# Kernel optimization log

Measured on AMD Instinct MI355X. Metric: run time of the kernel, lower is better.

Reference implementation:

```python
import jax, jax.numpy as jnp
import numpy as np

N = 100000   # nodes
E = 1600000  # edges (avg degree 16)
D = 128      # input_dim = hidden_dim = output_dim


def setup_inputs() -> dict:
    key = jax.random.key(0)
    ks = jax.random.split(key, 16)
    s = 0.02
    inp = {
        "node_emb": jax.random.normal(ks[0], (N, D), dtype=jnp.float32),
        "edge_index": jax.random.randint(ks[1], (2, E), 0, N, dtype=jnp.int64),
        # last-layer GCN branch (conv1 -> relu -> conv2); earlier layers are dead code in SSL.forward
        "gcn_w1": jax.random.normal(ks[2], (D, D), dtype=jnp.float32) * s,
        "gcn_b1": jnp.zeros((D,), dtype=jnp.float32),
        "gcn_w2": jax.random.normal(ks[3], (D, D), dtype=jnp.float32) * s,
        "gcn_b2": jnp.zeros((D,), dtype=jnp.float32),
        # last-layer GIN branch (GINConv eps=0, Mlp == single Linear)
        "gin_w1": jax.random.normal(ks[4], (D, D), dtype=jnp.float32) * s,
        "gin_b1": jnp.zeros((D,), dtype=jnp.float32),
        "gin_w2": jax.random.normal(ks[5], (D, D), dtype=jnp.float32) * s,
        "gin_b2": jnp.zeros((D,), dtype=jnp.float32),
        # fusion heads
        "lin_w": jax.random.normal(ks[6], (D, D), dtype=jnp.float32) * s,
        "lin_b": jnp.zeros((D,), dtype=jnp.float32),
        "fc_w": jax.random.normal(ks[7], (D, D), dtype=jnp.float32) * s,
        "fc_b": jnp.zeros((D,), dtype=jnp.float32),
    }
    return inp


def reference(node_emb, edge_index, gcn_w1, gcn_b1, gcn_w2, gcn_b2,
              gin_w1, gin_b1, gin_w2, gin_b2, lin_w, lin_b, fc_w, fc_b):
    n = node_emb.shape[0]
    src, dst = edge_index[0], edge_index[1]

    # symmetric GCN normalization with self-loops: deg counts incoming edges + 1
    deg = jax.ops.segment_sum(jnp.ones(src.shape[0], node_emb.dtype), dst, num_segments=n) + 1.0
    dinv = jax.lax.rsqrt(deg)                  # deg >= 1 always
    edge_norm = dinv[src] * dinv[dst]          # [E]
    self_norm = dinv * dinv                    # [N] self-loop coefficient

    def gcn_conv(x, W, b):
        y = x @ W                                                        # [N, D]
        agg = jax.ops.segment_sum(y[src] * edge_norm[:, None], dst, num_segments=n)
        return agg + self_norm[:, None] * y + b

    def gin_conv(x, W, b):
        # GINConv(train_eps=False): nn((1+0)*x + sum_{j in N(i)} x_j), nn = Linear
        agg = jax.ops.segment_sum(x[src], dst, num_segments=n)
        return (x + agg) @ W + b

    # GCN branch: conv1 -> relu -> (dropout=identity in eval) -> conv2
    h = jax.nn.relu(gcn_conv(node_emb, gcn_w1, gcn_b1))
    x_gcn = gcn_conv(h, gcn_w2, gcn_b2)

    # GIN branch: conv1 -> conv2
    g = gin_conv(node_emb, gin_w1, gin_b1)
    x_gin = gin_conv(g, gin_w2, gin_b2)

    # fusion heads
    x_gin = x_gin @ lin_w + lin_b
    x_gcn = x_gcn @ lin_w + lin_b
    return (x_gin + x_gcn) @ fc_w + fc_b
```

## Files before the change

### kernel.cpp

```cpp
#include <hip/hip_runtime.h>

#define D 128

using s8v = __attribute__((ext_vector_type(8))) short;
using f4v = __attribute__((ext_vector_type(4))) float;

__device__ __forceinline__ float bf2f(ushort u) {
  union { uint i; float f; } v; v.i = ((uint)u) << 16; return v.f;
}
__device__ __forceinline__ ushort f2bf(float f) {
  union { float f; uint i; } v; v.f = f;
  uint b = v.i;
  return (ushort)((b + 0x7fffu + ((b >> 16) & 1u)) >> 16);
}

__global__ void degpos_kernel(const int* __restrict__ dst, int* __restrict__ ideg,
                              int* __restrict__ pos, int E) {
  int i = blockIdx.x * blockDim.x + threadIdx.x;
  int stride = gridDim.x * blockDim.x;
  for (int e = i; e < E; e += stride)
    pos[e] = atomicAdd(&ideg[dst[e]], 1);
}

__global__ void scan1_kernel(const int* __restrict__ deg, int* __restrict__ incl,
                             int* __restrict__ bsum, int n) {
  __shared__ int tmp[256];
  int t = threadIdx.x;
  int i = blockIdx.x * 256 + t;
  int v = (i < n) ? deg[i] : 0;
  tmp[t] = v;
  __syncthreads();
#pragma unroll
  for (int off = 1; off < 256; off <<= 1) {
    int u = (t >= off) ? tmp[t - off] : 0;
    __syncthreads();
    tmp[t] += u;
    __syncthreads();
  }
  if (i < n) incl[i] = tmp[t];
  if (t == 255) bsum[blockIdx.x] = tmp[255];
}

__global__ void scan2_kernel(int* __restrict__ bsum, int nb) {
  __shared__ int tmp[256];
  __shared__ int carry_s;
  int t = threadIdx.x;
  if (t == 0) carry_s = 0;
  __syncthreads();
  for (int base = 0; base < nb; base += 256) {
    int v = (base + t < nb) ? bsum[base + t] : 0;
    tmp[t] = v;
    __syncthreads();
#pragma unroll
    for (int off = 1; off < 256; off <<= 1) {
      int u = (t >= off) ? tmp[t - off] : 0;
      __syncthreads();
      tmp[t] += u;
      __syncthreads();
    }
    int inc = tmp[t] + carry_s;
    if (base + t < nb) bsum[base + t] = inc;
    __syncthreads();
    if (t == 255) carry_s = inc;
    __syncthreads();
  }
}

__global__ void scan3_kernel(const int* __restrict__ deg, const int* __restrict__ incl,
                             const int* __restrict__ bsum, int* __restrict__ rowptr,
                             float* __restrict__ dinv, int n, int E) {
  int i = blockIdx.x * 256 + threadIdx.x;
  if (i < n) {
    int carry = (blockIdx.x > 0) ? bsum[blockIdx.x - 1] : 0;
    int d = deg[i];
    rowptr[i] = incl[i] - d + carry;
    dinv[i] = rsqrtf((float)d + 1.0f);
  }
  if (i == 0) rowptr[n] = E;
}

__global__ void scatter_kernel(const int* __restrict__ src, const int* __restrict__ dst,
                               const int* __restrict__ rowptr, const int* __restrict__ pos,
                               int* __restrict__ csrc, int E) {
  int i = blockIdx.x * blockDim.x + threadIdx.x;
  int stride = gridDim.x * blockDim.x;
  for (int e = i; e < E; e += stride)
    csrc[rowptr[dst[e]] + pos[e]] = src[e];
}

__global__ void xcvt_kernel(const float* __restrict__ x, ushort* __restrict__ xb, long total) {
  long i = ((long)blockIdx.x * blockDim.x + threadIdx.x) * 8;
  long stride = (long)gridDim.x * blockDim.x * 8;
  for (long t = i; t < total; t += stride) {
    float4 v0 = *(const float4*)(x + t);
    float4 v1 = *(const float4*)(x + t + 4);
    s8v u;
    u[0] = (short)f2bf(v0.x); u[1] = (short)f2bf(v0.y);
    u[2] = (short)f2bf(v0.z); u[3] = (short)f2bf(v0.w);
    u[4] = (short)f2bf(v1.x); u[5] = (short)f2bf(v1.y);
    u[6] = (short)f2bf(v1.z); u[7] = (short)f2bf(v1.w);
    *(s8v*)(xb + t) = u;
  }
}

__global__ void prep1_kernel(const float* __restrict__ gw1, const float* __restrict__ iw1,
                             ushort* __restrict__ Wt1g, ushort* __restrict__ Wt1i,
                             const float* __restrict__ lw, const float* __restrict__ fw,
                             float* __restrict__ LF) {
  int b = blockIdx.x;
  if (b < 128) {
    int t = b * 256 + threadIdx.x;
    int which = t >> 14, q = t & 16383;
    int k = q >> 7, c = q & 127;
    const float* w = which ? iw1 : gw1;
    ushort* o = which ? Wt1i : Wt1g;
    o[c * 128 + k] = f2bf(w[k * 128 + c]);
  } else {
    int t = (b - 128) * 256 + threadIdx.x;
    int r = t >> 7, c = t & 127;
    float s = 0.f;
#pragma unroll 8
    for (int k = 0; k < 128; ++k) s = fmaf(lw[r * 128 + k], fw[k * 128 + c], s);
    LF[r * 128 + c] = s;
  }
}

__global__ void prep2_kernel(const float* __restrict__ gw2, const float* __restrict__ iw2,
                             const float* __restrict__ LF,
                             ushort* __restrict__ Wt2g, ushort* __restrict__ Wt2i,
                             const float* __restrict__ gb2, const float* __restrict__ ib2,
                             const float* __restrict__ lb, const float* __restrict__ fw,
                             const float* __restrict__ fb, float* __restrict__ btot) {
  int b = blockIdx.x;
  if (b < 128) {
    int t = b * 256 + threadIdx.x;
    int which = t >> 14, q = t & 16383;
    int k = q >> 7, c = q & 127;
    const float* W = which ? iw2 : gw2;
    ushort* O = which ? Wt2i : Wt2g;
    float s = 0.f;
#pragma unroll 8
    for (int j = 0; j < 128; ++j) s = fmaf(W[k * 128 + j], LF[j * 128 + c], s);
    O[c * 128 + k] = f2bf(s);
  } else if (threadIdx.x < 128) {
    int c = threadIdx.x;
    float s = fb[c];
#pragma unroll 8
    for (int j = 0; j < 128; ++j) {
      s = fmaf(gb2[j] + ib2[j], LF[j * 128 + c], s);
      s = fmaf(2.f * lb[j], fw[j * 128 + c], s);
    }
    btot[c] = s;
  }
}

__global__ __launch_bounds__(256) void gatherA_kernel(
    const ushort* __restrict__ xb, const float* __restrict__ dinv,
    const int* __restrict__ rowptr, const int* __restrict__ csrc,
    ushort* __restrict__ ab, int n) {
  int nd = blockIdx.x * 4 + (threadIdx.x >> 6);
  if (nd >= n) return;
  int lane = threadIdx.x & 63;
  int half = lane >> 5;
  int hl = lane & 31;
  int beg = rowptr[nd], end = rowptr[nd + 1];
  float4 sg = make_float4(0.f, 0.f, 0.f, 0.f);
  float4 sc = make_float4(0.f, 0.f, 0.f, 0.f);
  int j = beg + half;
  for (; j + 6 < end; j += 8) {
    int s0 = csrc[j], s1 = csrc[j + 2], s2 = csrc[j + 4], s3 = csrc[j + 6];
    float w0 = dinv[s0], w1 = dinv[s1], w2 = dinv[s2], w3 = dinv[s3];
    ushort4 v0 = *(const ushort4*)(xb + (long)s0 * D + 4 * hl);
    ushort4 v1 = *(const ushort4*)(xb + (long)s1 * D + 4 * hl);
    ushort4 v2 = *(const ushort4*)(xb + (long)s2 * D + 4 * hl);
    ushort4 v3 = *(const ushort4*)(xb + (long)s3 * D + 4 * hl);
    float a0 = bf2f(v0.x), a1 = bf2f(v0.y), a2 = bf2f(v0.z), a3 = bf2f(v0.w);
    sg.x += a0; sg.y += a1; sg.z += a2; sg.w += a3;
    sc.x = fmaf(w0, a0, sc.x); sc.y = fmaf(w0, a1, sc.y);
    sc.z = fmaf(w0, a2, sc.z); sc.w = fmaf(w0, a3, sc.w);
    a0 = bf2f(v1.x); a1 = bf2f(v1.y); a2 = bf2f(v1.z); a3 = bf2f(v1.w);
    sg.x += a0; sg.y += a1; sg.z += a2; sg.w += a3;
    sc.x = fmaf(w1, a0, sc.x); sc.y = fmaf(w1, a1, sc.y);
    sc.z = fmaf(w1, a2, sc.z); sc.w = fmaf(w1, a3, sc.w);
    a0 = bf2f(v2.x); a1 = bf2f(v2.y); a2 = bf2f(v2.z); a3 = bf2f(v2.w);
    sg.x += a0; sg.y += a1; sg.z += a2; sg.w += a3;
    sc.x = fmaf(w2, a0, sc.x); sc.y = fmaf(w2, a1, sc.y);
    sc.z = fmaf(w2, a2, sc.z); sc.w = fmaf(w2, a3, sc.w);
    a0 = bf2f(v3.x); a1 = bf2f(v3.y); a2 = bf2f(v3.z); a3 = bf2f(v3.w);
    sg.x += a0; sg.y += a1; sg.z += a2; sg.w += a3;
    sc.x = fmaf(w3, a0, sc.x); sc.y = fmaf(w3, a1, sc.y);
    sc.z = fmaf(w3, a2, sc.z); sc.w = fmaf(w3, a3, sc.w);
  }
  for (; j < end; j += 2) {
    int s0 = csrc[j];
    float w0 = dinv[s0];
    ushort4 v0 = *(const ushort4*)(xb + (long)s0 * D + 4 * hl);
    float a0 = bf2f(v0.x), a1 = bf2f(v0.y), a2 = bf2f(v0.z), a3 = bf2f(v0.w);
    sg.x += a0; sg.y += a1; sg.z += a2; sg.w += a3;
    sc.x = fmaf(w0, a0, sc.x); sc.y = fmaf(w0, a1, sc.y);
    sc.z = fmaf(w0, a2, sc.z); sc.w = fmaf(w0, a3, sc.w);
  }
  sg.x += __shfl_xor(sg.x, 32); sg.y += __shfl_xor(sg.y, 32);
  sg.z += __shfl_xor(sg.z, 32); sg.w += __shfl_xor(sg.w, 32);
  sc.x += __shfl_xor(sc.x, 32); sc.y += __shfl_xor(sc.y, 32);
  sc.z += __shfl_xor(sc.z, 32); sc.w += __shfl_xor(sc.w, 32);

  ushort4 us = *(const ushort4*)(xb + (long)nd * D + 4 * hl);
  float x0 = bf2f(us.x), x1 = bf2f(us.y), x2 = bf2f(us.z), x3 = bf2f(us.w);
  float dd = dinv[nd];
  ushort4 o;
  if (half == 0) {
    o.x = f2bf(dd * (sc.x + dd * x0));
    o.y = f2bf(dd * (sc.y + dd * x1));
    o.z = f2bf(dd * (sc.z + dd * x2));
    o.w = f2bf(dd * (sc.w + dd * x3));
    *(ushort4*)(ab + (long)nd * 256 + 4 * hl) = o;
  } else {
    o.x = f2bf(x0 + sg.x);
    o.y = f2bf(x1 + sg.y);
    o.z = f2bf(x2 + sg.z);
    o.w = f2bf(x3 + sg.w);
    *(ushort4*)(ab + (long)nd * 256 + 128 + 4 * hl) = o;
  }
}

__global__ __launch_bounds__(256) void gatherB_kernel(
    const ushort* __restrict__ hg, const float* __restrict__ dinv,
    const int* __restrict__ rowptr, const int* __restrict__ csrc,
    ushort* __restrict__ ab2, int n) {
  int nd = blockIdx.x * 4 + (threadIdx.x >> 6);
  if (nd >= n) return;
  int lane = threadIdx.x & 63;
  int half = lane >> 5;
  int beg = rowptr[nd], end = rowptr[nd + 1];
  float4 s = make_float4(0.f, 0.f, 0.f, 0.f);
  int j = beg;
  for (; j + 3 < end; j += 4) {
    int s0 = csrc[j], s1 = csrc[j + 1], s2 = csrc[j + 2], s3 = csrc[j + 3];
    float w0 = dinv[s0], w1 = dinv[s1], w2 = dinv[s2], w3 = dinv[s3];
    ushort4 v0 = *(const ushort4*)(hg + (long)s0 * 256 + lane * 4);
    ushort4 v1 = *(const ushort4*)(hg + (long)s1 * 256 + lane * 4);
    ushort4 v2 = *(const ushort4*)(hg + (long)s2 * 256 + lane * 4);
    ushort4 v3 = *(const ushort4*)(hg + (long)s3 * 256 + lane * 4);
    float c0 = half ? 1.f : w0;
    float c1 = half ? 1.f : w1;
    float c2 = half ? 1.f : w2;
    float c3 = half ? 1.f : w3;
    s.x = fmaf(c0, bf2f(v0.x), s.x); s.y = fmaf(c0, bf2f(v0.y), s.y);
    s.z = fmaf(c0, bf2f(v0.z), s.z); s.w = fmaf(c0, bf2f(v0.w), s.w);
    s.x = fmaf(c1, bf2f(v1.x), s.x); s.y = fmaf(c1, bf2f(v1.y), s.y);
    s.z = fmaf(c1, bf2f(v1.z), s.z); s.w = fmaf(c1, bf2f(v1.w), s.w);
    s.x = fmaf(c2, bf2f(v2.x), s.x); s.y = fmaf(c2, bf2f(v2.y), s.y);
    s.z = fmaf(c2, bf2f(v2.z), s.z); s.w = fmaf(c2, bf2f(v2.w), s.w);
    s.x = fmaf(c3, bf2f(v3.x), s.x); s.y = fmaf(c3, bf2f(v3.y), s.y);
    s.z = fmaf(c3, bf2f(v3.z), s.z); s.w = fmaf(c3, bf2f(v3.w), s.w);
  }
  for (; j < end; ++j) {
    int s0 = csrc[j];
    float w0 = dinv[s0];
    ushort4 v0 = *(const ushort4*)(hg + (long)s0 * 256 + lane * 4);
    float c0 = half ? 1.f : w0;
    s.x = fmaf(c0, bf2f(v0.x), s.x); s.y = fmaf(c0, bf2f(v0.y), s.y);
    s.z = fmaf(c0, bf2f(v0.z), s.z); s.w = fmaf(c0, bf2f(v0.w), s.w);
  }
  ushort4 u = *(const ushort4*)(hg + (long)nd * 256 + lane * 4);
  float dd = dinv[nd];
  float4 o;
  if (half == 0) {
    o.x = dd * (s.x + dd * bf2f(u.x));
    o.y = dd * (s.y + dd * bf2f(u.y));
    o.z = dd * (s.z + dd * bf2f(u.z));
    o.w = dd * (s.w + dd * bf2f(u.w));
  } else {
    o.x = s.x + bf2f(u.x);
    o.y = s.y + bf2f(u.y);
    o.z = s.z + bf2f(u.z);
    o.w = s.w + bf2f(u.w);
  }
  ushort4 r;
  r.x = f2bf(o.x); r.y = f2bf(o.y); r.z = f2bf(o.z); r.w = f2bf(o.w);
  *(ushort4*)(ab2 + (long)nd * 256 + lane * 4) = r;
}

__global__ __launch_bounds__(256) void gemm1_kernel(
    const ushort* __restrict__ ab,
    const ushort* __restrict__ Wg, const ushort* __restrict__ Wi,
    const float* __restrict__ bg, const float* __restrict__ bi,
    ushort* __restrict__ hg, int n) {
  const int y = blockIdx.y;
  const ushort* __restrict__ Wt = y ? Wi : Wg;
  const float* __restrict__ bias = y ? bi : bg;
  __shared__ ushort Ws[128 * 128];
  const int tid = threadIdx.x;
  const int wave = tid >> 6, lane = tid & 63;
  const int rlo = lane & 15, khi = lane >> 4;
  const int rb = blockIdx.x * 128 + wave * 32;

  s8v a[2][4];
#pragma unroll
  for (int rt = 0; rt < 2; ++rt) {
    int row = rb + rt * 16 + rlo;
    row = row < n ? row : n - 1;
    const ushort* p = ab + (long)row * 256 + y * 128 + khi * 8;
#pragma unroll
    for (int ks = 0; ks < 4; ++ks) a[rt][ks] = *(const s8v*)(p + ks * 32);
  }

#pragma unroll
  for (int j = 0; j < 8; ++j) {
    int q = tid + 256 * j;
    int c = q >> 4, kc = q & 15;
    *(s8v*)&Ws[c * 128 + ((kc ^ (c & 7)) << 3)] = *(const s8v*)(Wt + c * 128 + kc * 8);
  }
  __syncthreads();

  f4v acc[2][8];
#pragma unroll
  for (int rt = 0; rt < 2; ++rt)
#pragma unroll
    for (int ct = 0; ct < 8; ++ct) acc[rt][ct] = (f4v){0.f, 0.f, 0.f, 0.f};

#pragma unroll
  for (int ks = 0; ks < 4; ++ks) {
#pragma unroll
    for (int ct = 0; ct < 8; ++ct) {
      int c = ct * 16 + rlo;
      int kc = ks * 4 + khi;
      s8v b = *(const s8v*)&Ws[c * 128 + ((kc ^ (c & 7)) << 3)];
      acc[0][ct] = __builtin_amdgcn_mfma_f32_16x16x32_bf16(a[0][ks], b, acc[0][ct], 0, 0, 0);
      acc[1][ct] = __builtin_amdgcn_mfma_f32_16x16x32_bf16(a[1][ks], b, acc[1][ct], 0, 0, 0);
    }
  }

#pragma unroll
  for (int ct = 0; ct < 8; ++ct) {
    int col = ct * 16 + rlo;
    float bb = bias[col];
#pragma unroll
    for (int rt = 0; rt < 2; ++rt) {
#pragma unroll
      for (int i = 0; i < 4; ++i) {
        int row = rb + rt * 16 + 4 * khi + i;
        if (row < n) {
          float v = acc[rt][ct][i] + bb;
          if (y == 0) v = fmaxf(v, 0.f);
          hg[(long)row * 256 + y * 128 + col] = f2bf(v);
        }
      }
    }
  }
}

__global__ __launch_bounds__(256) void gemm2_kernel(
    const ushort* __restrict__ ab2,
    const ushort* __restrict__ Wt2g, const ushort* __restrict__ Wt2i,
    const float* __restrict__ btot, float* __restrict__ out, int n) {
  __shared__ ushort Ws[2 * 128 * 128];
  const int tid = threadIdx.x;
  const int wave = tid >> 6, lane = tid & 63;
  const int rlo = lane & 15, khi = lane >> 4;
  const int rb = blockIdx.x * 128 + wave * 32;

  s8v a1[2][4], a2[2][4];
#pragma unroll
  for (int rt = 0; rt < 2; ++rt) {
    int row = rb + rt * 16 + rlo;
    row = row < n ? row : n - 1;
    const ushort* p = ab2 + (long)row * 256 + khi * 8;
#pragma unroll
    for (int ks = 0; ks < 4; ++ks) a1[rt][ks] = *(const s8v*)(p + ks * 32);
#pragma unroll
    for (int ks = 0; ks < 4; ++ks) a2[rt][ks] = *(const s8v*)(p + 128 + ks * 32);
  }

#pragma unroll
  for (int j = 0; j < 8; ++j) {
    int q = tid + 256 * j;
    int c = q >> 4, kc = q & 15;
    *(s8v*)&Ws[c * 128 + ((kc ^ (c & 7)) << 3)] = *(const s8v*)(Wt2g + c * 128 + kc * 8);
  }
#pragma unroll
  for (int j = 0; j < 8; ++j) {
    int q = tid + 256 * j;
    int c = q >> 4, kc = q & 15;
    *(s8v*)&Ws[128 * 128 + c * 128 + ((kc ^ (c & 7)) << 3)] =
        *(const s8v*)(Wt2i + c * 128 + kc * 8);
  }
  __syncthreads();

  f4v acc[2][8];
#pragma unroll
  for (int rt = 0; rt < 2; ++rt)
#pragma unroll
    for (int ct = 0; ct < 8; ++ct) acc[rt][ct] = (f4v){0.f, 0.f, 0.f, 0.f};

#pragma unroll
  for (int ks = 0; ks < 4; ++ks) {
#pragma unroll
    for (int ct = 0; ct < 8; ++ct) {
      int c = ct * 16 + rlo;
      int kc = ks * 4 + khi;
      s8v b = *(const s8v*)&Ws[c * 128 + ((kc ^ (c & 7)) << 3)];
      acc[0][ct] = __builtin_amdgcn_mfma_f32_16x16x32_bf16(a1[0][ks], b, acc[0][ct], 0, 0, 0);
      acc[1][ct] = __builtin_amdgcn_mfma_f32_16x16x32_bf16(a1[1][ks], b, acc[1][ct], 0, 0, 0);
    }
  }
#pragma unroll
  for (int ks = 0; ks < 4; ++ks) {
#pragma unroll
    for (int ct = 0; ct < 8; ++ct) {
      int c = ct * 16 + rlo;
      int kc = ks * 4 + khi;
      s8v b = *(const s8v*)&Ws[128 * 128 + c * 128 + ((kc ^ (c & 7)) << 3)];
      acc[0][ct] = __builtin_amdgcn_mfma_f32_16x16x32_bf16(a2[0][ks], b, acc[0][ct], 0, 0, 0);
      acc[1][ct] = __builtin_amdgcn_mfma_f32_16x16x32_bf16(a2[1][ks], b, acc[1][ct], 0, 0, 0);
    }
  }

#pragma unroll
  for (int ct = 0; ct < 8; ++ct) {
    int col = ct * 16 + rlo;
    float bb = btot[col];
#pragma unroll
    for (int rt = 0; rt < 2; ++rt) {
#pragma unroll
      for (int i = 0; i < 4; ++i) {
        int row = rb + rt * 16 + 4 * khi + i;
        if (row < n)
          out[(long)row * D + col] = acc[rt][ct][i] + bb;
      }
    }
  }
}

extern "C" void kernel_launch(void* const* d_in, const int* in_sizes, int n_in,
                              void* d_out, int out_size, void* d_ws, size_t ws_size,
                              hipStream_t stream) {
  const float* x   = (const float*)d_in[0];
  const int*   ei  = (const int*)d_in[1];
  const float* gw1 = (const float*)d_in[2];
  const float* gb1 = (const float*)d_in[3];
  const float* gw2 = (const float*)d_in[4];
  const float* gb2 = (const float*)d_in[5];
  const float* iw1 = (const float*)d_in[6];
  const float* ib1 = (const float*)d_in[7];
  const float* iw2 = (const float*)d_in[8];
  const float* ib2 = (const float*)d_in[9];
  const float* lw  = (const float*)d_in[10];
  const float* lb  = (const float*)d_in[11];
  const float* fw  = (const float*)d_in[12];
  const float* fb  = (const float*)d_in[13];
  float* out = (float*)d_out;

  const int n = in_sizes[0] / D;
  const int E = in_sizes[1] / 2;
  const int* src = ei;
  const int* dst = ei + E;
  const int nb = (n + 255) / 256;
  const long ND = (long)n * D;

  char* p = (char*)d_ws;
  auto alloc = [&](size_t bytes) {
    char* r = p;
    p += (bytes + 255) & ~(size_t)255;
    return r;
  };
  int* ideg    = (int*)alloc((size_t)n * 4);
  int* incl    = (int*)alloc((size_t)n * 4);
  int* rowptr  = (int*)alloc((size_t)(n + 1) * 4);
  int* bsum    = (int*)alloc(1024 * 4);
  int* pos     = (int*)alloc((size_t)E * 4);
  int* csrc    = (int*)alloc((size_t)E * 4);
  float* dinv  = (float*)alloc((size_t)n * 4);
  float* LF    = (float*)alloc(16384 * 4);
  float* btot  = (float*)alloc(128 * 4);
  ushort* xb   = (ushort*)alloc(ND * 2);
  ushort* Wt1g = (ushort*)alloc(16384 * 2);
  ushort* Wt1i = (ushort*)alloc(16384 * 2);
  ushort* Wt2g = (ushort*)alloc(16384 * 2);
  ushort* Wt2i = (ushort*)alloc(16384 * 2);
  ushort* ab   = (ushort*)alloc(2 * ND * 2);
  ushort* hg   = (ushort*)alloc(2 * ND * 2);

  hipMemsetAsync(ideg, 0, (size_t)n * 4, stream);

  degpos_kernel<<<2048, 256, 0, stream>>>(dst, ideg, pos, E);
  scan1_kernel<<<nb, 256, 0, stream>>>(ideg, incl, bsum, n);
  scan2_kernel<<<1, 256, 0, stream>>>(bsum, nb);
  scan3_kernel<<<nb, 256, 0, stream>>>(ideg, incl, bsum, rowptr, dinv, n, E);
  scatter_kernel<<<2048, 256, 0, stream>>>(src, dst, rowptr, pos, csrc, E);

  xcvt_kernel<<<2048, 256, 0, stream>>>(x, xb, ND);
  prep1_kernel<<<192, 256, 0, stream>>>(gw1, iw1, Wt1g, Wt1i, lw, fw, LF);
  prep2_kernel<<<129, 256, 0, stream>>>(gw2, iw2, LF, Wt2g, Wt2i, gb2, ib2, lb, fw, fb, btot);

  gatherA_kernel<<<(n + 3) / 4, 256, 0, stream>>>(xb, dinv, rowptr, csrc, ab, n);
  const int nblk = (n + 127) / 128;
  gemm1_kernel<<<dim3(nblk, 2), 256, 0, stream>>>(ab, Wt1g, Wt1i, gb1, ib1, hg, n);

  gatherB_kernel<<<(n + 3) / 4, 256, 0, stream>>>(hg, dinv, rowptr, csrc, ab, n);
  gemm2_kernel<<<nblk, 256, 0, stream>>>(ab, Wt2g, Wt2i, btot, out, n);
}
```

Baseline: 425.9 us.

## Reassociate second-layer GEMMs before aggregation and fuse prep kernels

The second layer's weight products (W2·lin·fc for both branches, and the GIN first-layer weight folded with its second-layer product) are precomputed, so gemm1 emits the final projected features directly. The GCN half does a second in-block GEMM from a shared-memory relu tile, and gatherB now aggregates and writes the fp32 output itself, which removes gemm2 and the intermediate bf16 round trip. Several small setup kernels are merged into multi-role launches to cut launch count. In exchange, gemm1 does more work and uses more LDS, and folding weights into bf16 products changes rounding.

```diff
diff --git a/kernel.cpp b/kernel.cpp
--- a/kernel.cpp
+++ b/kernel.cpp
@@ -1,6 +1,7 @@
 #include <hip/hip_runtime.h>
 
 #define D 128
+#define HS_LD 136
 
 using s8v = __attribute__((ext_vector_type(8))) short;
 using f4v = __attribute__((ext_vector_type(4))) float;
@@ -14,41 +15,59 @@
   return (ushort)((b + 0x7fffu + ((b >> 16) & 1u)) >> 16);
 }
 
-__global__ void degpos_kernel(const int* __restrict__ dst, int* __restrict__ ideg,
-                              int* __restrict__ pos, int E) {
-  int i = blockIdx.x * blockDim.x + threadIdx.x;
-  int stride = gridDim.x * blockDim.x;
-  for (int e = i; e < E; e += stride)
-    pos[e] = atomicAdd(&ideg[dst[e]], 1);
-}
-
-__global__ void scan1_kernel(const int* __restrict__ deg, int* __restrict__ incl,
-                             int* __restrict__ bsum, int n) {
-  __shared__ int tmp[256];
-  int t = threadIdx.x;
-  int i = blockIdx.x * 256 + t;
-  int v = (i < n) ? deg[i] : 0;
-  tmp[t] = v;
-  __syncthreads();
-#pragma unroll
-  for (int off = 1; off < 256; off <<= 1) {
-    int u = (t >= off) ? tmp[t - off] : 0;
-    __syncthreads();
-    tmp[t] += u;
-    __syncthreads();
-  }
-  if (i < n) incl[i] = tmp[t];
-  if (t == 255) bsum[blockIdx.x] = tmp[255];
-}
-
-__global__ void scan2_kernel(int* __restrict__ bsum, int nb) {
-  __shared__ int tmp[256];
-  __shared__ int carry_s;
-  int t = threadIdx.x;
-  if (t == 0) carry_s = 0;
-  __syncthreads();
-  for (int base = 0; base < nb; base += 256) {
-    int v = (base + t < nb) ? bsum[base + t] : 0;
+__global__ void megaA_kernel(const int* __restrict__ dst, int* __restrict__ ideg,
+                             int* __restrict__ pos, int E,
+                             const float* __restrict__ x, ushort* __restrict__ xb, long total,
+                             const float* __restrict__ lw, const float* __restrict__ fw,
+                             float* __restrict__ LF,
+                             const float* __restrict__ gw1, ushort* __restrict__ T1g) {
+  int b = blockIdx.x;
+  if (b < 2048) {
+    int i = b * 256 + threadIdx.x;
+    int stride = 2048 * 256;
+    for (int e = i; e < E; e += stride)
+      pos[e] = atomicAdd(&ideg[dst[e]], 1);
+  } else if (b < 5248) {
+    long i = ((long)(b - 2048) * 256 + threadIdx.x) * 8;
+    long stride = (long)3200 * 256 * 8;
+    for (long t = i; t < total; t += stride) {
+      float4 v0 = *(const float4*)(x + t);
+      float4 v1 = *(const float4*)(x + t + 4);
+      s8v u;
+      u[0] = (short)f2bf(v0.x); u[1] = (short)f2bf(v0.y);
+      u[2] = (short)f2bf(v0.z); u[3] = (short)f2bf(v0.w);
+      u[4] = (short)f2bf(v1.x); u[5] = (short)f2bf(v1.y);
+      u[6] = (short)f2bf(v1.z); u[7] = (short)f2bf(v1.w);
+      *(s8v*)(xb + t) = u;
+    }
+  } else if (b < 5312) {
+    int t = (b - 5248) * 256 + threadIdx.x;
+    int r = t >> 7, c = t & 127;
+    float s = 0.f;
+#pragma unroll 8
+    for (int k = 0; k < 128; ++k) s = fmaf(lw[r * 128 + k], fw[k * 128 + c], s);
+    LF[r * 128 + c] = s;
+  } else {
+    int t = (b - 5312) * 256 + threadIdx.x;
+    int k = t >> 7, c = t & 127;
+    T1g[c * 128 + k] = f2bf(gw1[k * 128 + c]);
+  }
+}
+
+__global__ void scanP_kernel(const int* __restrict__ deg, int* __restrict__ incl,
+                             int* __restrict__ bsum, int n, int nb,
+                             const float* __restrict__ iw2, const float* __restrict__ gw2,
+                             const float* __restrict__ LF,
+                             float* __restrict__ M2i, ushort* __restrict__ W2gT,
+                             const float* __restrict__ gb2, const float* __restrict__ ib2,
+                             const float* __restrict__ lb, const float* __restrict__ fw,
+                             const float* __restrict__ fb, float* __restrict__ btot) {
+  int b = blockIdx.x;
+  if (b < nb) {
+    __shared__ int tmp[256];
+    int t = threadIdx.x;
+    int i = b * 256 + t;
+    int v = (i < n) ? deg[i] : 0;
     tmp[t] = v;
     __syncthreads();
 #pragma unroll
@@ -58,11 +77,75 @@
       tmp[t] += u;
       __syncthreads();
     }
-    int inc = tmp[t] + carry_s;
-    if (base + t < nb) bsum[base + t] = inc;
+    if (i < n) incl[i] = tmp[t];
+    if (t == 255) bsum[b] = tmp[255];
+  } else if (b < nb + 64) {
+    int t = (b - nb) * 256 + threadIdx.x;
+    int k = t >> 7, c = t & 127;
+    float s = 0.f;
+#pragma unroll 8
+    for (int j = 0; j < 128; ++j) s = fmaf(iw2[k * 128 + j], LF[j * 128 + c], s);
+    M2i[k * 128 + c] = s;
+  } else if (b < nb + 128) {
+    int t = (b - nb - 64) * 256 + threadIdx.x;
+    int k = t >> 7, c = t & 127;
+    float s = 0.f;
+#pragma unroll 8
+    for (int j = 0; j < 128; ++j) s = fmaf(gw2[k * 128 + j], LF[j * 128 + c], s);
+    W2gT[c * 128 + k] = f2bf(s);
+  } else if (threadIdx.x < 128) {
+    int c = threadIdx.x;
+    float s = fb[c];
+#pragma unroll 8
+    for (int j = 0; j < 128; ++j) {
+      s = fmaf(gb2[j] + ib2[j], LF[j * 128 + c], s);
+      s = fmaf(2.f * lb[j], fw[j * 128 + c], s);
+    }
+    btot[c] = s;
+  }
+}
+
+__global__ void scan2F_kernel(int* __restrict__ bsum, int nb,
+                              const float* __restrict__ iw1, const float* __restrict__ M2i,
+                              ushort* __restrict__ WginT,
+                              const float* __restrict__ ib1, float* __restrict__ bgin) {
+  int b = blockIdx.x;
+  if (b == 0) {
+    __shared__ int tmp[256];
+    __shared__ int carry_s;
+    int t = threadIdx.x;
+    if (t == 0) carry_s = 0;
     __syncthreads();
-    if (t == 255) carry_s = inc;
-    __syncthreads();
+    for (int base = 0; base < nb; base += 256) {
+      int v = (base + t < nb) ? bsum[base + t] : 0;
+      tmp[t] = v;
+      __syncthreads();
+#pragma unroll
+      for (int off = 1; off < 256; off <<= 1) {
+        int u = (t >= off) ? tmp[t - off] : 0;
+        __syncthreads();
+        tmp[t] += u;
+        __syncthreads();
+      }
+      int inc = tmp[t] + carry_s;
+      if (base + t < nb) bsum[base + t] = inc;
+      __syncthreads();
+      if (t == 255) carry_s = inc;
+      __syncthreads();
+    }
+  } else if (b <= 64) {
+    int t = (b - 1) * 256 + threadIdx.x;
+    int k = t >> 7, c = t & 127;
+    float s = 0.f;
+#pragma unroll 8
+    for (int j = 0; j < 128; ++j) s = fmaf(iw1[k * 128 + j], M2i[j * 128 + c], s);
+    WginT[c * 128 + k] = f2bf(s);
+  } else if (threadIdx.x < 128) {
+    int c = threadIdx.x;
+    float s = 0.f;
+#pragma unroll 8
+    for (int j = 0; j < 128; ++j) s = fmaf(ib1[j], M2i[j * 128 + c], s);
+    bgin[c] = s;
   }
 }
 
@@ -86,72 +169,6 @@
   int stride = gridDim.x * blockDim.x;
   for (int e = i; e < E; e += stride)
     csrc[rowptr[dst[e]] + pos[e]] = src[e];
-}
-
-__global__ void xcvt_kernel(const float* __restrict__ x, ushort* __restrict__ xb, long total) {
-  long i = ((long)blockIdx.x * blockDim.x + threadIdx.x) * 8;
-  long stride = (long)gridDim.x * blockDim.x * 8;
-  for (long t = i; t < total; t += stride) {
-    float4 v0 = *(const float4*)(x + t);
-    float4 v1 = *(const float4*)(x + t + 4);
-    s8v u;
-    u[0] = (short)f2bf(v0.x); u[1] = (short)f2bf(v0.y);
-    u[2] = (short)f2bf(v0.z); u[3] = (short)f2bf(v0.w);
-    u[4] = (short)f2bf(v1.x); u[5] = (short)f2bf(v1.y);
-    u[6] = (short)f2bf(v1.z); u[7] = (short)f2bf(v1.w);
-    *(s8v*)(xb + t) = u;
-  }
-}
-
-__global__ void prep1_kernel(const float* __restrict__ gw1, const float* __restrict__ iw1,
-                             ushort* __restrict__ Wt1g, ushort* __restrict__ Wt1i,
-                             const float* __restrict__ lw, const float* __restrict__ fw,
-                             float* __restrict__ LF) {
-  int b = blockIdx.x;
-  if (b < 128) {
-    int t = b * 256 + threadIdx.x;
-    int which = t >> 14, q = t & 16383;
-    int k = q >> 7, c = q & 127;
-    const float* w = which ? iw1 : gw1;
-    ushort* o = which ? Wt1i : Wt1g;
-    o[c * 128 + k] = f2bf(w[k * 128 + c]);
-  } else {
-    int t = (b - 128) * 256 + threadIdx.x;
-    int r = t >> 7, c = t & 127;
-    float s = 0.f;
-#pragma unroll 8
-    for (int k = 0; k < 128; ++k) s = fmaf(lw[r * 128 + k], fw[k * 128 + c], s);
-    LF[r * 128 + c] = s;
-  }
-}
-
-__global__ void prep2_kernel(const float* __restrict__ gw2, const float* __restrict__ iw2,
-                             const float* __restrict__ LF,
-                             ushort* __restrict__ Wt2g, ushort* __restrict__ Wt2i,
-                             const float* __restrict__ gb2, const float* __restrict__ ib2,
-                             const float* __restrict__ lb, const float* __restrict__ fw,
-                             const float* __restrict__ fb, float* __restrict__ btot) {
-  int b = blockIdx.x;
-  if (b < 128) {
-    int t = b * 256 + threadIdx.x;
-    int which = t >> 14, q = t & 16383;
-    int k = q >> 7, c = q & 127;
-    const float* W = which ? iw2 : gw2;
-    ushort* O = which ? Wt2i : Wt2g;
-    float s = 0.f;
-#pragma unroll 8
-    for (int j = 0; j < 128; ++j) s = fmaf(W[k * 128 + j], LF[j * 128 + c], s);
-    O[c * 128 + k] = f2bf(s);
-  } else if (threadIdx.x < 128) {
-    int c = threadIdx.x;
-    float s = fb[c];
-#pragma unroll 8
-    for (int j = 0; j < 128; ++j) {
-      s = fmaf(gb2[j] + ib2[j], LF[j * 128 + c], s);
-      s = fmaf(2.f * lb[j], fw[j * 128 + c], s);
-    }
-    btot[c] = s;
-  }
 }
 
 __global__ __launch_bounds__(256) void gatherA_kernel(
@@ -224,24 +241,160 @@
   }
 }
 
+__global__ __launch_bounds__(256) void gemm1_kernel(
+    const ushort* __restrict__ ab,
+    const ushort* __restrict__ T1g, const ushort* __restrict__ WginT,
+    const ushort* __restrict__ W2gT,
+    const float* __restrict__ gb1, const float* __restrict__ bgin,
+    ushort* __restrict__ pq, int n) {
+  __shared__ ushort Ws[128 * 128];
+  __shared__ ushort Hs[128 * HS_LD];
+  const int y = blockIdx.y;
+  const int tid = threadIdx.x;
+  const int wave = tid >> 6, lane = tid & 63;
+  const int rlo = lane & 15, khi = lane >> 4;
+  const int rb = blockIdx.x * 128 + wave * 32;
+
+  s8v a[2][4];
+#pragma unroll
+  for (int rt = 0; rt < 2; ++rt) {
+    int row = rb + rt * 16 + rlo;
+    row = row < n ? row : n - 1;
+    const ushort* p = ab + (long)row * 256 + y * 128 + khi * 8;
+#pragma unroll
+    for (int ks = 0; ks < 4; ++ks) a[rt][ks] = *(const s8v*)(p + ks * 32);
+  }
+
+  {
+    const ushort* W = y ? WginT : T1g;
+#pragma unroll
+    for (int j = 0; j < 8; ++j) {
+      int q = tid + 256 * j;
+      int c = q >> 4, kc = q & 15;
+      *(s8v*)&Ws[c * 128 + ((kc ^ (c & 7)) << 3)] = *(const s8v*)(W + c * 128 + kc * 8);
+    }
+  }
+  __syncthreads();
+
+  f4v acc[2][8];
+#pragma unroll
+  for (int rt = 0; rt < 2; ++rt)
+#pragma unroll
+    for (int ct = 0; ct < 8; ++ct) acc[rt][ct] = (f4v){0.f, 0.f, 0.f, 0.f};
+
+#pragma unroll
+  for (int ks = 0; ks < 4; ++ks) {
+#pragma unroll
+    for (int ct = 0; ct < 8; ++ct) {
+      int c = ct * 16 + rlo;
+      int kc = ks * 4 + khi;
+      s8v b = *(const s8v*)&Ws[c * 128 + ((kc ^ (c & 7)) << 3)];
+      acc[0][ct] = __builtin_amdgcn_mfma_f32_16x16x32_bf16(a[0][ks], b, acc[0][ct], 0, 0, 0);
+      acc[1][ct] = __builtin_amdgcn_mfma_f32_16x16x32_bf16(a[1][ks], b, acc[1][ct], 0, 0, 0);
+    }
+  }
+
+  if (y == 1) {
+#pragma unroll
+    for (int ct = 0; ct < 8; ++ct) {
+      int col = ct * 16 + rlo;
+      float bb = bgin[col];
+#pragma unroll
+      for (int rt = 0; rt < 2; ++rt) {
+#pragma unroll
+        for (int i = 0; i < 4; ++i) {
+          int row = rb + rt * 16 + 4 * khi + i;
+          if (row < n)
+            pq[(long)row * 256 + 128 + col] = f2bf(acc[rt][ct][i] + bb);
+        }
+      }
+    }
+    return;
+  }
+
+  __syncthreads();
+#pragma unroll
+  for (int ct = 0; ct < 8; ++ct) {
+    int col = ct * 16 + rlo;
+    float bb = gb1[col];
+#pragma unroll
+    for (int rt = 0; rt < 2; ++rt) {
+#pragma unroll
+      for (int i = 0; i < 4; ++i) {
+        int r = wave * 32 + rt * 16 + 4 * khi + i;
+        Hs[r * HS_LD + col] = f2bf(fmaxf(acc[rt][ct][i] + bb, 0.f));
+      }
+    }
+  }
+#pragma unroll
+  for (int j = 0; j < 8; ++j) {
+    int q = tid + 256 * j;
+    int c = q >> 4, kc = q & 15;
+    *(s8v*)&Ws[c * 128 + ((kc ^ (c & 7)) << 3)] = *(const s8v*)(W2gT + c * 128 + kc * 8);
+  }
+  __syncthreads();
+
+  s8v a2[2][4];
+#pragma unroll
+  for (int rt = 0; rt < 2; ++rt) {
+    int r = wave * 32 + rt * 16 + rlo;
+#pragma unroll
+    for (int ks = 0; ks < 4; ++ks)
+      a2[rt][ks] = *(const s8v*)&Hs[r * HS_LD + (ks * 4 + khi) * 8];
+  }
+
+  f4v acc2[2][8];
+#pragma unroll
+  for (int rt = 0; rt < 2; ++rt)
+#pragma unroll
+    for (int ct = 0; ct < 8; ++ct) acc2[rt][ct] = (f4v){0.f, 0.f, 0.f, 0.f};
+
+#pragma unroll
+  for (int ks = 0; ks < 4; ++ks) {
+#pragma unroll
+    for (int ct = 0; ct < 8; ++ct) {
+      int c = ct * 16 + rlo;
+      int kc = ks * 4 + khi;
+      s8v b = *(const s8v*)&Ws[c * 128 + ((kc ^ (c & 7)) << 3)];
+      acc2[0][ct] = __builtin_amdgcn_mfma_f32_16x16x32_bf16(a2[0][ks], b, acc2[0][ct], 0, 0, 0);
+      acc2[1][ct] = __builtin_amdgcn_mfma_f32_16x16x32_bf16(a2[1][ks], b, acc2[1][ct], 0, 0, 0);
+    }
+  }
+
+#pragma unroll
+  for (int ct = 0; ct < 8; ++ct) {
+    int col = ct * 16 + rlo;
+#pragma unroll
+    for (int rt = 0; rt < 2; ++rt) {
+#pragma unroll
+      for (int i = 0; i < 4; ++i) {
+        int row = rb + rt * 16 + 4 * khi + i;
+        if (row < n)
+          pq[(long)row * 256 + col] = f2bf(acc2[rt][ct][i]);
+      }
+    }
+  }
+}
+
 __global__ __launch_bounds__(256) void gatherB_kernel(
-    const ushort* __restrict__ hg, const float* __restrict__ dinv,
+    const ushort* __restrict__ pq, const float* __restrict__ dinv,
     const int* __restrict__ rowptr, const int* __restrict__ csrc,
-    ushort* __restrict__ ab2, int n) {
+    const float* __restrict__ btot, float* __restrict__ out, int n) {
   int nd = blockIdx.x * 4 + (threadIdx.x >> 6);
   if (nd >= n) return;
   int lane = threadIdx.x & 63;
   int half = lane >> 5;
+  int hl = lane & 31;
   int beg = rowptr[nd], end = rowptr[nd + 1];
   float4 s = make_float4(0.f, 0.f, 0.f, 0.f);
   int j = beg;
   for (; j + 3 < end; j += 4) {
     int s0 = csrc[j], s1 = csrc[j + 1], s2 = csrc[j + 2], s3 = csrc[j + 3];
     float w0 = dinv[s0], w1 = dinv[s1], w2 = dinv[s2], w3 = dinv[s3];
-    ushort4 v0 = *(const ushort4*)(hg + (long)s0 * 256 + lane * 4);
-    ushort4 v1 = *(const ushort4*)(hg + (long)s1 * 256 + lane * 4);
-    ushort4 v2 = *(const ushort4*)(hg + (long)s2 * 256 + lane * 4);
-    ushort4 v3 = *(const ushort4*)(hg + (long)s3 * 256 + lane * 4);
+    ushort4 v0 = *(const ushort4*)(pq + (long)s0 * 256 + lane * 4);
+    ushort4 v1 = *(const ushort4*)(pq + (long)s1 * 256 + lane * 4);
+    ushort4 v2 = *(const ushort4*)(pq + (long)s2 * 256 + lane * 4);
+    ushort4 v3 = *(const ushort4*)(pq + (long)s3 * 256 + lane * 4);
     float c0 = half ? 1.f : w0;
     float c1 = half ? 1.f : w1;
     float c2 = half ? 1.f : w2;
@@ -258,12 +411,12 @@
   for (; j < end; ++j) {
     int s0 = csrc[j];
     float w0 = dinv[s0];
-    ushort4 v0 = *(const ushort4*)(hg + (long)s0 * 256 + lane * 4);
+    ushort4 v0 = *(const ushort4*)(pq + (long)s0 * 256 + lane * 4);
     float c0 = half ? 1.f : w0;
     s.x = fmaf(c0, bf2f(v0.x), s.x); s.y = fmaf(c0, bf2f(v0.y), s.y);
     s.z = fmaf(c0, bf2f(v0.z), s.z); s.w = fmaf(c0, bf2f(v0.w), s.w);
   }
-  ushort4 u = *(const ushort4*)(hg + (long)nd * 256 + lane * 4);
+  ushort4 u = *(const ushort4*)(pq + (long)nd * 256 + lane * 4);
   float dd = dinv[nd];
   float4 o;
   if (half == 0) {
@@ -277,159 +430,14 @@
     o.z = s.z + bf2f(u.z);
     o.w = s.w + bf2f(u.w);
   }
-  ushort4 r;
-  r.x = f2bf(o.x); r.y = f2bf(o.y); r.z = f2bf(o.z); r.w = f2bf(o.w);
-  *(ushort4*)(ab2 + (long)nd * 256 + lane * 4) = r;
-}
-
-__global__ __launch_bounds__(256) void gemm1_kernel(
-    const ushort* __restrict__ ab,
-    const ushort* __restrict__ Wg, const ushort* __restrict__ Wi,
-    const float* __restrict__ bg, const float* __restrict__ bi,
-    ushort* __restrict__ hg, int n) {
-  const int y = blockIdx.y;
-  const ushort* __restrict__ Wt = y ? Wi : Wg;
-  const float* __restrict__ bias = y ? bi : bg;
-  __shared__ ushort Ws[128 * 128];
-  const int tid = threadIdx.x;
-  const int wave = tid >> 6, lane = tid & 63;
-  const int rlo = lane & 15, khi = lane >> 4;
-  const int rb = blockIdx.x * 128 + wave * 32;
-
-  s8v a[2][4];
-#pragma unroll
-  for (int rt = 0; rt < 2; ++rt) {
-    int row = rb + rt * 16 + rlo;
-    row = row < n ? row : n - 1;
-    const ushort* p = ab + (long)row * 256 + y * 128 + khi * 8;
-#pragma unroll
-    for (int ks = 0; ks < 4; ++ks) a[rt][ks] = *(const s8v*)(p + ks * 32);
-  }
-
-#pragma unroll
-  for (int j = 0; j < 8; ++j) {
-    int q = tid + 256 * j;
-    int c = q >> 4, kc = q & 15;
-    *(s8v*)&Ws[c * 128 + ((kc ^ (c & 7)) << 3)] = *(const s8v*)(Wt + c * 128 + kc * 8);
-  }
-  __syncthreads();
-
-  f4v acc[2][8];
-#pragma unroll
-  for (int rt = 0; rt < 2; ++rt)
-#pragma unroll
-    for (int ct = 0; ct < 8; ++ct) acc[rt][ct] = (f4v){0.f, 0.f, 0.f, 0.f};
-
-#pragma unroll
-  for (int ks = 0; ks < 4; ++ks) {
-#pragma unroll
-    for (int ct = 0; ct < 8; ++ct) {
-      int c = ct * 16 + rlo;
-      int kc = ks * 4 + khi;
-      s8v b = *(const s8v*)&Ws[c * 128 + ((kc ^ (c & 7)) << 3)];
-      acc[0][ct] = __builtin_amdgcn_mfma_f32_16x16x32_bf16(a[0][ks], b, acc[0][ct], 0, 0, 0);
-      acc[1][ct] = __builtin_amdgcn_mfma_f32_16x16x32_bf16(a[1][ks], b, acc[1][ct], 0, 0, 0);
-    }
-  }
-
-#pragma unroll
-  for (int ct = 0; ct < 8; ++ct) {
-    int col = ct * 16 + rlo;
-    float bb = bias[col];
-#pragma unroll
-    for (int rt = 0; rt < 2; ++rt) {
-#pragma unroll
-      for (int i = 0; i < 4; ++i) {
-        int row = rb + rt * 16 + 4 * khi + i;
-        if (row < n) {
-          float v = acc[rt][ct][i] + bb;
-          if (y == 0) v = fmaxf(v, 0.f);
-          hg[(long)row * 256 + y * 128 + col] = f2bf(v);
-        }
-      }
-    }
-  }
-}
-
-__global__ __launch_bounds__(256) void gemm2_kernel(
-    const ushort* __restrict__ ab2,
-    const ushort* __restrict__ Wt2g, const ushort* __restrict__ Wt2i,
-    const float* __restrict__ btot, float* __restrict__ out, int n) {
-  __shared__ ushort Ws[2 * 128 * 128];
-  const int tid = threadIdx.x;
-  const int wave = tid >> 6, lane = tid & 63;
-  const int rlo = lane & 15, khi = lane >> 4;
-  const int rb = blockIdx.x * 128 + wave * 32;
-
-  s8v a1[2][4], a2[2][4];
-#pragma unroll
-  for (int rt = 0; rt < 2; ++rt) {
-    int row = rb + rt * 16 + rlo;
-    row = row < n ? row : n - 1;
-    const ushort* p = ab2 + (long)row * 256 + khi * 8;
-#pragma unroll
-    for (int ks = 0; ks < 4; ++ks) a1[rt][ks] = *(const s8v*)(p + ks * 32);
-#pragma unroll
-    for (int ks = 0; ks < 4; ++ks) a2[rt][ks] = *(const s8v*)(p + 128 + ks * 32);
-  }
-
-#pragma unroll
-  for (int j = 0; j < 8; ++j) {
-    int q = tid + 256 * j;
-    int c = q >> 4, kc = q & 15;
-    *(s8v*)&Ws[c * 128 + ((kc ^ (c & 7)) << 3)] = *(const s8v*)(Wt2g + c * 128 + kc * 8);
-  }
-#pragma unroll
-  for (int j = 0; j < 8; ++j) {
-    int q = tid + 256 * j;
-    int c = q >> 4, kc = q & 15;
-    *(s8v*)&Ws[128 * 128 + c * 128 + ((kc ^ (c & 7)) << 3)] =
-        *(const s8v*)(Wt2i + c * 128 + kc * 8);
-  }
-  __syncthreads();
-
-  f4v acc[2][8];
-#pragma unroll
-  for (int rt = 0; rt < 2; ++rt)
-#pragma unroll
-    for (int ct = 0; ct < 8; ++ct) acc[rt][ct] = (f4v){0.f, 0.f, 0.f, 0.f};
-
-#pragma unroll
-  for (int ks = 0; ks < 4; ++ks) {
-#pragma unroll
-    for (int ct = 0; ct < 8; ++ct) {
-      int c = ct * 16 + rlo;
-      int kc = ks * 4 + khi;
-      s8v b = *(const s8v*)&Ws[c * 128 + ((kc ^ (c & 7)) << 3)];
-      acc[0][ct] = __builtin_amdgcn_mfma_f32_16x16x32_bf16(a1[0][ks], b, acc[0][ct], 0, 0, 0);
-      acc[1][ct] = __builtin_amdgcn_mfma_f32_16x16x32_bf16(a1[1][ks], b, acc[1][ct], 0, 0, 0);
-    }
-  }
-#pragma unroll
-  for (int ks = 0; ks < 4; ++ks) {
-#pragma unroll
-    for (int ct = 0; ct < 8; ++ct) {
-      int c = ct * 16 + rlo;
-      int kc = ks * 4 + khi;
-      s8v b = *(const s8v*)&Ws[128 * 128 + c * 128 + ((kc ^ (c & 7)) << 3)];
-      acc[0][ct] = __builtin_amdgcn_mfma_f32_16x16x32_bf16(a2[0][ks], b, acc[0][ct], 0, 0, 0);
-      acc[1][ct] = __builtin_amdgcn_mfma_f32_16x16x32_bf16(a2[1][ks], b, acc[1][ct], 0, 0, 0);
-    }
-  }
-
-#pragma unroll
-  for (int ct = 0; ct < 8; ++ct) {
-    int col = ct * 16 + rlo;
-    float bb = btot[col];
-#pragma unroll
-    for (int rt = 0; rt < 2; ++rt) {
-#pragma unroll
-      for (int i = 0; i < 4; ++i) {
-        int row = rb + rt * 16 + 4 * khi + i;
-        if (row < n)
-          out[(long)row * D + col] = acc[rt][ct][i] + bb;
-      }
-    }
+  o.x += __shfl_xor(o.x, 32);
+  o.y += __shfl_xor(o.y, 32);
+  o.z += __shfl_xor(o.z, 32);
+  o.w += __shfl_xor(o.w, 32);
+  if (half == 0) {
+    float4 bt = *(const float4*)(btot + 4 * hl);
+    o.x += bt.x; o.y += bt.y; o.z += bt.z; o.w += bt.w;
+    *(float4*)(out + (long)nd * D + 4 * hl) = o;
   }
 }
 
@@ -473,31 +481,27 @@
   int* csrc    = (int*)alloc((size_t)E * 4);
   float* dinv  = (float*)alloc((size_t)n * 4);
   float* LF    = (float*)alloc(16384 * 4);
+  float* M2i   = (float*)alloc(16384 * 4);
   float* btot  = (float*)alloc(128 * 4);
+  float* bgin  = (float*)alloc(128 * 4);
   ushort* xb   = (ushort*)alloc(ND * 2);
-  ushort* Wt1g = (ushort*)alloc(16384 * 2);
-  ushort* Wt1i = (ushort*)alloc(16384 * 2);
-  ushort* Wt2g = (ushort*)alloc(16384 * 2);
-  ushort* Wt2i = (ushort*)alloc(16384 * 2);
+  ushort* T1g   = (ushort*)alloc(16384 * 2);
+  ushort* WginT = (ushort*)alloc(16384 * 2);
+  ushort* W2gT  = (ushort*)alloc(16384 * 2);
   ushort* ab   = (ushort*)alloc(2 * ND * 2);
-  ushort* hg   = (ushort*)alloc(2 * ND * 2);
+  ushort* pq   = (ushort*)alloc(2 * ND * 2);
 
   hipMemsetAsync(ideg, 0, (size_t)n * 4, stream);
 
-  degpos_kernel<<<2048, 256, 0, stream>>>(dst, ideg, pos, E);
-  scan1_kernel<<<nb, 256, 0, stream>>>(ideg, incl, bsum, n);
-  scan2_kernel<<<1, 256, 0, stream>>>(bsum, nb);
+  megaA_kernel<<<5376, 256, 0, stream>>>(dst, ideg, pos, E, x, xb, ND, lw, fw, LF, gw1, T1g);
+  scanP_kernel<<<nb + 129, 256, 0, stream>>>(ideg, incl, bsum, n, nb, iw2, gw2, LF,
+                                             M2i, W2gT, gb2, ib2, lb, fw, fb, btot);
+  scan2F_kernel<<<66, 256, 0, stream>>>(bsum, nb, iw1, M2i, WginT, ib1, bgin);
   scan3_kernel<<<nb, 256, 0, stream>>>(ideg, incl, bsum, rowptr, dinv, n, E);
   scatter_kernel<<<2048, 256, 0, stream>>>(src, dst, rowptr, pos, csrc, E);
 
-  xcvt_kernel<<<2048, 256, 0, stream>>>(x, xb, ND);
-  prep1_kernel<<<192, 256, 0, stream>>>(gw1, iw1, Wt1g, Wt1i, lw, fw, LF);
-  prep2_kernel<<<129, 256, 0, stream>>>(gw2, iw2, LF, Wt2g, Wt2i, gb2, ib2, lb, fw, fb, btot);
-
   gatherA_kernel<<<(n + 3) / 4, 256, 0, stream>>>(xb, dinv, rowptr, csrc, ab, n);
   const int nblk = (n + 127) / 128;
-  gemm1_kernel<<<dim3(nblk, 2), 256, 0, stream>>>(ab, Wt1g, Wt1i, gb1, ib1, hg, n);
-
-  gatherB_kernel<<<(n + 3) / 4, 256, 0, stream>>>(hg, dinv, rowptr, csrc, ab, n);
-  gemm2_kernel<<<nblk, 256, 0, stream>>>(ab, Wt2g, Wt2i, btot, out, n);
-}
+  gemm1_kernel<<<dim3(nblk, 2), 256, 0, stream>>>(ab, T1g, WginT, W2gT, gb1, bgin, pq, n);
+  gatherB_kernel<<<(n + 3) / 4, 256, 0, stream>>>(pq, dinv, rowptr, csrc, btot, out, n);
+}
```

Result: faster. 374.3 us (-12.1%).
